# Kernel optimization log

Measured on AMD Instinct MI355X. Metric: run time of the kernel, lower is better.

The kernel has to match this reference:

```python
import jax, jax.numpy as jnp
import numpy as np

D_MODEL = 1024
D_STATE = 128
D_CONV = 4
EXPAND = 2
HEADDIM = 64
NGROUPS = 1
CHUNK = 256
D_INNER = EXPAND * D_MODEL          # 2048
NHEADS = D_INNER // HEADDIM         # 32
D_IN_PROJ = 2 * D_INNER + 2 * NGROUPS * D_STATE + NHEADS  # 4384
CONV_DIM = D_INNER + 2 * NGROUPS * D_STATE                # 2304
BATCH, SEQLEN = 2, 2048


def rmsnorm(x, w, eps=1e-6):
    ms = jnp.mean(x * x, axis=-1, keepdims=True)
    return w * (x * jax.lax.rsqrt(ms + eps))


def layernorm(x, eps=1e-5):
    mu = jnp.mean(x, axis=-1, keepdims=True)
    var = jnp.mean((x - mu) ** 2, axis=-1, keepdims=True)
    return (x - mu) * jax.lax.rsqrt(var + eps)


def activation_quant(x):
    # int8-style fake quant with STE, scale differentiable (matches torch)
    amax = jnp.clip(jnp.max(jnp.abs(x), axis=-1, keepdims=True), 1e-5, None)
    scale = 127.0 / amax
    q = jnp.clip(jnp.round(x * scale), -128, 127)
    return (jax.lax.stop_gradient(q - x * scale) + x * scale) / scale


def weight_quant(w):
    # ternary {-1,0,1}; note: NOT rescaled by scale (matches the triton kernel)
    scale = jnp.clip(jnp.mean(jnp.abs(w)), 1e-5, None)
    wq = jnp.clip(jnp.round(w / scale), -1.0, 1.0)
    return w + jax.lax.stop_gradient(wq - w)  # STE: identity grad


def bitlinear(x, w):
    return activation_quant(layernorm(x)) @ weight_quant(w).T


def segsum(x):
    # x: [..., T] -> [..., T, T] lower-triangular cumulative segment sums
    T = x.shape[-1]
    cs = jnp.cumsum(x, axis=-1)
    ss = cs[..., :, None] - cs[..., None, :]
    mask = jnp.tril(jnp.ones((T, T), dtype=bool))
    return jnp.where(mask, ss, -jnp.inf)


def ssd(u, a, B, C, chunk):
    # u: b l h p (= x*dt); a: b l h (= A*dt); B, C: b l h n (per-head)
    b, l, h, p = u.shape
    n = B.shape[-1]
    c = l // chunk
    u = u.reshape(b, c, chunk, h, p)
    a = a.reshape(b, c, chunk, h).transpose(0, 3, 1, 2)   # b h c s
    B = B.reshape(b, c, chunk, h, n)
    C = C.reshape(b, c, chunk, h, n)
    a_cs = jnp.cumsum(a, axis=-1)                          # b h c s
    L = jnp.exp(segsum(a))                                 # b h c s s
    Y_diag = jnp.einsum('bclhn,bcshn,bhcls,bcshp->bclhp', C, B, L, u)
    decay_states = jnp.exp(a_cs[..., -1:] - a_cs)          # b h c s
    states = jnp.einsum('bclhn,bhcl,bclhp->bchpn', B, decay_states, u)
    a_chunk = jnp.pad(a_cs[..., -1], ((0, 0), (0, 0), (1, 0)))  # b h (c+1)
    decay_chunk = jnp.exp(segsum(a_chunk))                 # b h (c+1) (c+1)
    states = jnp.concatenate([jnp.zeros_like(states[:, :1]), states], axis=1)
    new_states = jnp.einsum('bhzc,bchpn->bzhpn', decay_chunk, states)
    prev_states = new_states[:, :-1]                       # state entering each chunk
    Y_off = jnp.einsum('bclhn,bchpn,bhcl->bclhp', C, prev_states, jnp.exp(a_cs))
    return (Y_diag + Y_off).reshape(b, l, h, p)


def setup_inputs() -> dict:
    key = jax.random.key(0)
    ks = jax.random.split(key, 6)
    hidden_states = jax.random.normal(ks[0], (BATCH, SEQLEN, D_MODEL), jnp.float32)
    in_proj_w = jax.random.normal(ks[1], (D_IN_PROJ, D_MODEL), jnp.float32) / np.sqrt(D_MODEL).astype(np.float32)
    out_proj_w = jax.random.normal(ks[2], (D_MODEL, D_INNER), jnp.float32) / np.sqrt(D_INNER).astype(np.float32)
    conv_w = jax.random.normal(ks[3], (CONV_DIM, D_CONV), jnp.float32) * 0.1
    conv_b = jnp.zeros((CONV_DIM,), jnp.float32)
    A_log = jnp.log(jnp.arange(1, NHEADS + 1, dtype=jnp.float32))
    Dp = jnp.ones((NHEADS,), jnp.float32)
    dt_min, dt_max, dt_floor = 1e-3, 1e-1, 1e-4
    inv_dt = jnp.exp(jax.random.uniform(ks[4], (NHEADS,)) * (np.log(dt_max) - np.log(dt_min)) + np.log(dt_min))
    inv_dt = jnp.clip(inv_dt, dt_floor, None)
    dt_bias = inv_dt + jnp.log(-jnp.expm1(-inv_dt))
    norm_w = jnp.ones((D_MODEL,), jnp.float32)
    out_norm_w = jnp.ones((D_INNER,), jnp.float32)
    return dict(hidden_states=hidden_states, norm_w=norm_w, in_proj_w=in_proj_w,
                conv_w=conv_w, conv_b=conv_b, A_log=A_log, Dp=Dp, dt_bias=dt_bias,
                out_norm_w=out_norm_w, out_proj_w=out_proj_w)


def reference(hidden_states, norm_w, in_proj_w, conv_w, conv_b, A_log, Dp, dt_bias, out_norm_w, out_proj_w):
    b, l, _ = hidden_states.shape
    h = rmsnorm(hidden_states, norm_w)
    zxbcdt = bitlinear(h, in_proj_w)                       # b l (2*d_inner + 2*g*n + h)
    z = zxbcdt[..., :D_INNER]
    xBC = zxbcdt[..., D_INNER:D_INNER + CONV_DIM]
    dt = zxbcdt[..., D_INNER + CONV_DIM:]                  # b l h
    # causal depthwise conv1d (kernel D_CONV) + silu
    xp = jnp.pad(xBC, ((0, 0), (D_CONV - 1, 0), (0, 0)))
    conv = sum(xp[:, k:k + l, :] * conv_w[:, k] for k in range(D_CONV)) + conv_b
    xBC = jax.nn.silu(conv)
    x = xBC[..., :D_INNER].reshape(b, l, NHEADS, HEADDIM)
    Bm = xBC[..., D_INNER:D_INNER + NGROUPS * D_STATE].reshape(b, l, NGROUPS, D_STATE)
    Cm = xBC[..., D_INNER + NGROUPS * D_STATE:].reshape(b, l, NGROUPS, D_STATE)
    hpg = NHEADS // NGROUPS
    Bh = jnp.repeat(Bm, hpg, axis=2)                       # b l h n
    Ch = jnp.repeat(Cm, hpg, axis=2)
    dt = jax.nn.softplus(dt + dt_bias)                     # dt_softplus=True
    A = -jnp.exp(A_log)
    y = ssd(x * dt[..., None], dt * A, Bh, Ch, CHUNK)      # b l h p
    y = y + x * Dp[None, None, :, None]                    # D skip
    y = y * jax.nn.silu(z).reshape(b, l, NHEADS, HEADDIM)  # z gate
    y = rmsnorm(y.reshape(b, l, D_INNER), out_norm_w)
    out = bitlinear(y, out_proj_w)
    return hidden_states + out
```

## Files before the change

### kernel.cpp

```cpp
#include <hip/hip_runtime.h>
#include <stdint.h>
#include <stddef.h>
#include <math.h>

#define TOKS 4096
#define DM   1024
#define DIP  4384
#define DI   2048
#define CVD  2304
#define NH   32
#define HD   64
#define DST  128
#define NCH  8
#define CHK  256

typedef int v4i  __attribute__((ext_vector_type(4)));
typedef int v16i __attribute__((ext_vector_type(16)));
typedef short s8v __attribute__((ext_vector_type(8)));
typedef float f16v __attribute__((ext_vector_type(16)));
typedef unsigned short ushort_t;

static const size_t OFF_ZX    = 0;
static const size_t OFF_SX    = OFF_ZX + (size_t)TOKS*DIP*4;
static const size_t OFF_ST    = OFF_SX + (size_t)TOKS*CVD*4;
static const size_t OFF_YG    = OFF_ST + (size_t)512*HD*DST*4;
static const size_t OFF_Q1    = OFF_YG + (size_t)TOKS*DI*4;
static const size_t OFF_Q2    = OFF_Q1 + (size_t)TOKS*DM;
static const size_t OFF_WQ1   = OFF_Q2 + (size_t)TOKS*DI;
static const size_t OFF_WQ2   = OFF_WQ1 + (size_t)DIP*DM;
static const size_t OFF_RS1   = OFF_WQ2 + (size_t)DM*DI;
static const size_t OFF_RS2   = OFF_RS1 + (size_t)TOKS*4;
static const size_t OFF_DT    = OFF_RS2 + (size_t)TOKS*4;
static const size_t OFF_ACS   = OFF_DT + (size_t)TOKS*NH*4;
static const size_t OFF_CSUM  = OFF_ACS + (size_t)512*CHK*8;
static const size_t OFF_PART  = OFF_CSUM + 512*8;
static const size_t OFF_WSC   = OFF_PART + 1024*8;
static const size_t OFF_BH    = OFF_WSC + 64;
static const size_t OFF_BL    = OFF_BH  + (size_t)TOKS*128*2;
static const size_t OFF_CHG   = OFF_BL  + (size_t)TOKS*128*2;
static const size_t OFF_CLG   = OFF_CHG + (size_t)TOKS*128*2;
static const size_t OFF_GRAM  = OFF_CLG + (size_t)TOKS*128*2;
static const size_t OFF_UTH   = OFF_GRAM + (size_t)16*256*256*4;
static const size_t OFF_UTL   = OFF_UTH + (size_t)512*64*256*2;
static const size_t OFF_PH    = OFF_UTL + (size_t)512*64*256*2;
static const size_t OFF_PL    = OFF_PH  + (size_t)512*64*128*2;

__device__ __forceinline__ ushort_t f2bf(float x) {
  union { float f; unsigned int u; } v; v.f = x;
  unsigned int r = v.u + 0x7FFFu + ((v.u >> 16) & 1u);
  return (ushort_t)(r >> 16);
}
__device__ __forceinline__ float bf2f(ushort_t h) {
  union { unsigned int u; float f; } v; v.u = ((unsigned int)h) << 16;
  return v.f;
}

__device__ __forceinline__ double bsumd(double v, double* sb) {
#pragma unroll
  for (int o = 32; o; o >>= 1) v += __shfl_down(v, o);
  int lane = threadIdx.x & 63, w = threadIdx.x >> 6;
  __syncthreads();
  if (lane == 0) sb[w] = v;
  __syncthreads();
  return sb[0] + sb[1] + sb[2] + sb[3];
}
__device__ __forceinline__ double bmaxd(double v, double* sb) {
#pragma unroll
  for (int o = 32; o; o >>= 1) v = fmax(v, __shfl_down(v, o));
  int lane = threadIdx.x & 63, w = threadIdx.x >> 6;
  __syncthreads();
  if (lane == 0) sb[w] = v;
  __syncthreads();
  return fmax(fmax(sb[0], sb[1]), fmax(sb[2], sb[3]));
}
__device__ __forceinline__ void bsum3d(double& a, double& b, double& c, double* sb) {
#pragma unroll
  for (int o = 32; o; o >>= 1) {
    a += __shfl_down(a, o);
    b += __shfl_down(b, o);
    c += __shfl_down(c, o);
  }
  int lane = threadIdx.x & 63, w = threadIdx.x >> 6;
  __syncthreads();
  if (lane == 0) { sb[w * 3 + 0] = a; sb[w * 3 + 1] = b; sb[w * 3 + 2] = c; }
  __syncthreads();
  a = sb[0] + sb[3] + sb[6] + sb[9];
  b = sb[1] + sb[4] + sb[7] + sb[10];
  c = sb[2] + sb[5] + sb[8] + sb[11];
}

__global__ void __launch_bounds__(256) k_absmean(const float* __restrict__ w, int n, double* __restrict__ part) {
  double s = 0.0;
  for (int i = blockIdx.x * 256 + threadIdx.x; i < n; i += 512 * 256) s += (double)fabsf(w[i]);
  __shared__ double sb[4];
  s = bsumd(s, sb);
  if (threadIdx.x == 0) part[blockIdx.x] = s;
}

__global__ void __launch_bounds__(256) k_wscale(const double* __restrict__ part, double* __restrict__ wsc, int n1, int n2) {
  __shared__ double sb[4];
  double s = part[threadIdx.x] + part[threadIdx.x + 256];
  double t1 = bsumd(s, sb);
  __syncthreads();
  s = part[512 + threadIdx.x] + part[512 + threadIdx.x + 256];
  double t2 = bsumd(s, sb);
  if (threadIdx.x == 0) {
    wsc[0] = fmax(t1 / (double)n1, 1e-5);
    wsc[1] = fmax(t2 / (double)n2, 1e-5);
  }
}

__global__ void __launch_bounds__(256) k_tern(const float* __restrict__ w, int n, const double* __restrict__ wsc, int which, int8_t* __restrict__ out) {
  int i = blockIdx.x * 256 + threadIdx.x;
  if (i < n) {
    double sc = wsc[which];
    double q = fmin(fmax(rint((double)w[i] / sc), -1.0), 1.0);
    out[i] = (int8_t)q;
  }
}

template <int D>
__global__ void __launch_bounds__(256) k_normquant(const float* __restrict__ in, const float* __restrict__ w,
                                                   int8_t* __restrict__ q, float* __restrict__ rs) {
  constexpr int E = D / 256;
  int t = blockIdx.x, tid = threadIdx.x;
  const float* row = in + (size_t)t * D;
  __shared__ double sb[12];
  double y[E];
  double s0 = 0.0, s1 = 0.0, s2 = 0.0;
#pragma unroll
  for (int i = 0; i < E; i++) {
    double xv = (double)row[tid + 256 * i];
    double wv = (double)w[tid + 256 * i];
    s0 += xv * xv;
    double yy = wv * xv;
    y[i] = yy;
    s1 += yy;
    s2 += yy * yy;
  }
  bsum3d(s0, s1, s2, sb);
  double rr = 1.0 / sqrt(s0 / (double)D + 1e-6);
  double mu = rr * (s1 / (double)D);
  double var = rr * rr * (s2 / (double)D) - mu * mu;
  double rv = 1.0 / sqrt(var + 1e-5);
  double M = 0.0;
#pragma unroll
  for (int i = 0; i < E; i++) { y[i] = y[i] * rr - mu; M = fmax(M, fabs(y[i])); }
  M = bmaxd(M, sb);
  double am = fmax(M * rv, 1e-5);
  double sc = 127.0 / am;
#pragma unroll
  for (int i = 0; i < E; i++) {
    double qq = fmin(fmax(rint(y[i] * rv * sc), -128.0), 127.0);
    q[(size_t)t * D + tid + 256 * i] = (int8_t)qq;
  }
  if (tid == 0) rs[t] = (float)(am / 127.0);
}

__global__ void __launch_bounds__(256, 3) k_gemm_mfma(const int8_t* __restrict__ A, const int8_t* __restrict__ W,
                                                      const float* __restrict__ rs, const float* __restrict__ addend,
                                                      float* __restrict__ out, int M, int N, int K) {
  __shared__ int8_t Al[128 * 80];
  __shared__ int8_t Bl[128 * 80];
  int m0 = blockIdx.x * 128, n0 = blockIdx.y * 128;
  int t = threadIdx.x;
  int w = t >> 6, lane = t & 63;
  int wm = w >> 1, wn = w & 1;
  int l31 = lane & 31, lh = lane >> 5;

  v16i acc[2][2] = {};

  for (int k0 = 0; k0 < K; k0 += 64) {
    __syncthreads();
#pragma unroll
    for (int it = 0; it < 2; ++it) {
      int c = t + 256 * it;
      int row = c >> 2, kc = (c & 3) * 16;
      int4 av = *(const int4*)(A + (size_t)(m0 + row) * K + k0 + kc);
      *(int4*)(Al + row * 80 + kc) = av;
      int4 bv;
      if (n0 + row < N) bv = *(const int4*)(W + (size_t)(n0 + row) * K + k0 + kc);
      else { bv.x = bv.y = bv.z = bv.w = 0; }
      *(int4*)(Bl + row * 80 + kc) = bv;
    }
    __syncthreads();
#pragma unroll
    for (int ks = 0; ks < 2; ++ks) {
      v4i af[2], bf[2];
#pragma unroll
      for (int tm = 0; tm < 2; ++tm)
        af[tm] = *(const v4i*)(Al + (wm * 64 + tm * 32 + l31) * 80 + ks * 32 + lh * 16);
#pragma unroll
      for (int tn = 0; tn < 2; ++tn)
        bf[tn] = *(const v4i*)(Bl + (wn * 64 + tn * 32 + l31) * 80 + ks * 32 + lh * 16);
#pragma unroll
      for (int tm = 0; tm < 2; ++tm)
#pragma unroll
        for (int tn = 0; tn < 2; ++tn)
          acc[tm][tn] = __builtin_amdgcn_mfma_i32_32x32x32_i8(af[tm], bf[tn], acc[tm][tn], 0, 0, 0);
    }
  }

#pragma unroll
  for (int tm = 0; tm < 2; ++tm)
#pragma unroll
    for (int tn = 0; tn < 2; ++tn) {
      int n = n0 + wn * 64 + tn * 32 + l31;
      if (n < N) {
#pragma unroll
        for (int r = 0; r < 16; ++r) {
          int mrel = (r & 3) + 8 * (r >> 2) + 4 * lh;
          int m = m0 + wm * 64 + tm * 32 + mrel;
          float v = rs[m] * (float)acc[tm][tn][r];
          if (addend) v += addend[(size_t)m * N + n];
          out[(size_t)m * N + n] = v;
        }
      }
    }
}

__global__ void __launch_bounds__(256) k_conv(const float* __restrict__ zx, const float* __restrict__ cw,
                                              const float* __restrict__ cb, float* __restrict__ sx,
                                              ushort_t* __restrict__ bh2, ushort_t* __restrict__ bl2,
                                              ushort_t* __restrict__ ch2, ushort_t* __restrict__ cl2) {
  int c = blockIdx.x * 256 + threadIdx.x;
  int t = blockIdx.y;
  int b = t >> 11, l = t & 2047;
  float acc = cb[c];
#pragma unroll
  for (int k = 0; k < 4; k++) {
    int li = l - 3 + k;
    if (li >= 0) acc = fmaf(zx[(size_t)(b * 2048 + li) * DIP + DI + c], cw[c * 4 + k], acc);
  }
  float val = acc / (1.f + expf(-acc));
  sx[(size_t)t * CVD + c] = val;
  if (c >= DI) {
    int idx = c - DI;
    ushort_t hh = f2bf(val);
    ushort_t ll = f2bf(val - bf2f(hh));
    int bc = t >> 8, lt = (t >> 5) & 7, l31 = t & 31;
    int n = idx & 127;
    int ks = n >> 4, lhf = (n >> 3) & 1, j = n & 7;
    size_t o = ((((size_t)(bc * 8 + lt) * 8 + ks) * 2 + lhf) * 32 + l31) * 8 + j;
    if (idx < 128) { bh2[o] = hh; bl2[o] = ll; }
    else           { ch2[o] = hh; cl2[o] = ll; }
  }
}

__global__ void __launch_bounds__(256) k_cumsum(const float* __restrict__ zx, const float* __restrict__ dt_bias,
                                                const float* __restrict__ A_log, float* __restrict__ dtv,
                                                double* __restrict__ acs, double* __restrict__ csum) {
  int bid = blockIdx.x;
  int h = bid & 31, bc = bid >> 5;
  int s = threadIdx.x;
  int tok = bc * 256 + s;
  float x = zx[(size_t)tok * DIP + (DI + CVD) + h] + dt_bias[h];
  float dt = fmaxf(x, 0.f) + log1pf(expf(-fabsf(x)));
  dtv[(size_t)tok * 32 + h] = dt;
  double negA = -exp((double)A_log[h]);
  double a = (double)dt * negA;
  __shared__ double buf[256];
  buf[s] = a;
  __syncthreads();
  for (int o = 1; o < 256; o <<= 1) {
    double add = (s >= o) ? buf[s - o] : 0.0;
    __syncthreads();
    buf[s] += add;
    __syncthreads();
  }
  acs[(size_t)bid * 256 + s] = buf[s];
  if (s == 255) csum[bid] = buf[s];
}

__global__ void __launch_bounds__(256) k_gram(const ushort_t* __restrict__ bh2, const ushort_t* __restrict__ bl2,
                                              const ushort_t* __restrict__ ch2, const ushort_t* __restrict__ cl2,
                                              float* __restrict__ gr2) {
  int blk = blockIdx.x;
  int bc = blk >> 3, lt = blk & 7;
  int t = threadIdx.x;
  int w = t >> 6, lane = t & 63;
  int l31 = lane & 31, lhf = lane >> 5;
  __shared__ float Gl[4][32 * 36];

  s8v ch[8], cl[8];
#pragma unroll
  for (int ks = 0; ks < 8; ++ks) {
    size_t ca = ((((size_t)(bc * 8 + lt) * 8 + ks) * 2 + lhf) * 32 + l31) * 8;
    ch[ks] = *(const s8v*)(ch2 + ca);
    cl[ks] = *(const s8v*)(cl2 + ca);
  }
  for (int st = w; st <= lt; st += 4) {
    f16v acc = {};
#pragma unroll
    for (int ks = 0; ks < 8; ++ks) {
      size_t ba = ((((size_t)(bc * 8 + st) * 8 + ks) * 2 + lhf) * 32 + l31) * 8;
      s8v bh = *(const s8v*)(bh2 + ba);
      s8v bl = *(const s8v*)(bl2 + ba);
      acc = __builtin_amdgcn_mfma_f32_32x32x16_bf16(ch[ks], bh, acc, 0, 0, 0);
      acc = __builtin_amdgcn_mfma_f32_32x32x16_bf16(ch[ks], bl, acc, 0, 0, 0);
      acc = __builtin_amdgcn_mfma_f32_32x32x16_bf16(cl[ks], bh, acc, 0, 0, 0);
    }
#pragma unroll
    for (int rr = 0; rr < 16; ++rr) {
      int lrow = (rr & 3) + 8 * (rr >> 2) + 4 * lhf;
      Gl[w][lrow * 36 + l31] = acc[rr];
    }
#pragma unroll
    for (int i2 = 0; i2 < 2; ++i2) {
      int idx = i2 * 2 + lhf;
      int k2g = idx >> 1, lhf2 = idx & 1;
      size_t gb = ((((size_t)(bc * 8 + lt) * 8 + st) * 2 + k2g) * 2 + lhf2) * 256 + l31 * 8;
      float4 a = *(const float4*)(&Gl[w][l31 * 36 + k2g * 16 + lhf2 * 8]);
      float4 b = *(const float4*)(&Gl[w][l31 * 36 + k2g * 16 + lhf2 * 8 + 4]);
      *(float4*)(gr2 + gb) = a;
      *(float4*)(gr2 + gb + 4) = b;
    }
  }
}

__global__ void __launch_bounds__(256) k_prepuT(const float* __restrict__ sx, const float* __restrict__ dtv,
                                                ushort_t* __restrict__ uth2, ushort_t* __restrict__ utl2) {
  int r = blockIdx.x;
  int h = r & 31, bc = r >> 5;
  int t = threadIdx.x;
  __shared__ float Xs[64 * 68];
  __shared__ float dts[64];
  for (int slab = 0; slab < 4; ++slab) {
    int s0 = slab * 64;
    if (slab) __syncthreads();
    if (t < 64) dts[t] = dtv[(size_t)(bc * 256 + s0 + t) * 32 + h];
    {
      int s = t >> 2, pg = (t & 3) * 16;
      const float* xr = sx + (size_t)(bc * 256 + s0 + s) * CVD + h * 64 + pg;
      float* dst = &Xs[s * 68 + pg];
#pragma unroll
      for (int i = 0; i < 4; ++i)
        *(float4*)(dst + i * 4) = *(const float4*)(xr + i * 4);
    }
    __syncthreads();
#pragma unroll
    for (int half = 0; half < 2; ++half) {
      int it = t + half * 256;
      int l31 = it & 31, g = it >> 5;
      int stl = g >> 3, k2 = (g >> 2) & 1, pt = (g >> 1) & 1, lhf = g & 1;
      int p = pt * 32 + l31;
      int sb = stl * 32 + k2 * 16 + lhf * 8;
      union { int4 q; ushort_t e[8]; } H, L;
#pragma unroll
      for (int j = 0; j < 8; ++j) {
        float f = Xs[(sb + j) * 68 + p] * dts[sb + j];
        ushort_t hh = f2bf(f);
        H.e[j] = hh;
        L.e[j] = f2bf(f - bf2f(hh));
      }
      int st = slab * 2 + stl;
      size_t base = (((((size_t)r * 8 + st) * 2 + k2) * 2 + pt) * 2 + lhf) * 256 + l31 * 8;
      *(int4*)(uth2 + base) = H.q;
      *(int4*)(utl2 + base) = L.q;
    }
  }
}

__global__ void __launch_bounds__(256, 4) k_states2(const float* __restrict__ sx, const float* __restrict__ dtv,
                                                    const double* __restrict__ acs, const double* __restrict__ csum,
                                                    float* __restrict__ states) {
  int r = blockIdx.x;
  int h = r & 31, bc = r >> 5;
  int t = threadIdx.x, tx = t & 15, ty = t >> 4;
  __shared__ float du[64 * 68];
  double last = csum[r];
  float acc[4][8] = {};
  for (int s0 = 0; s0 < 256; s0 += 64) {
    __syncthreads();
    {
      int s = t >> 2, pg = (t & 3) * 16;
      int tok = bc * 256 + s0 + s;
      float w = expf((float)(last - acs[(size_t)r * 256 + s0 + s])) * dtv[(size_t)tok * 32 + h];
      const float* xr = sx + (size_t)tok * CVD + h * 64 + pg;
      float* dst = &du[s * 68 + pg];
#pragma unroll
      for (int i = 0; i < 4; i++) {
        float4 v = *(const float4*)(xr + i * 4);
        v.x *= w; v.y *= w; v.z *= w; v.w *= w;
        *(float4*)(dst + i * 4) = v;
      }
    }
    __syncthreads();
#pragma unroll 4
    for (int s = 0; s < 64; s++) {
      int tok = bc * 256 + s0 + s;
      const float* br = sx + (size_t)tok * CVD + DI + ty * 8;
      float4 b0 = *(const float4*)(br);
      float4 b1 = *(const float4*)(br + 4);
      float4 d4 = *(const float4*)(&du[s * 68 + tx * 4]);
      float dd[4] = {d4.x, d4.y, d4.z, d4.w};
      float bv[8] = {b0.x, b0.y, b0.z, b0.w, b1.x, b1.y, b1.z, b1.w};
#pragma unroll
      for (int i = 0; i < 4; i++)
#pragma unroll
        for (int j = 0; j < 8; j++) acc[i][j] = fmaf(dd[i], bv[j], acc[i][j]);
    }
  }
  size_t base = (size_t)r * (HD * DST);
#pragma unroll
  for (int i = 0; i < 4; i++) {
    float4 v0, v1;
    v0.x = acc[i][0]; v0.y = acc[i][1]; v0.z = acc[i][2]; v0.w = acc[i][3];
    v1.x = acc[i][4]; v1.y = acc[i][5]; v1.z = acc[i][6]; v1.w = acc[i][7];
    *(float4*)(states + base + (size_t)(tx * 4 + i) * DST + ty * 8) = v0;
    *(float4*)(states + base + (size_t)(tx * 4 + i) * DST + ty * 8 + 4) = v1;
  }
}

__global__ void __launch_bounds__(256) k_chunkscan(float* __restrict__ states, const double* __restrict__ csum,
                                                   ushort_t* __restrict__ ph2, ushort_t* __restrict__ pl2) {
  int idx = blockIdx.x * 256 + threadIdx.x;
  int n = idx & 127, p = (idx >> 7) & 63, h = (idx >> 13) & 31, b = idx >> 18;
  int ks = n >> 4, lhf = (n >> 3) & 1, j = n & 7, pt = p >> 5, l31 = p & 31;
  float Nv = 0.f;
  for (int c = 0; c < 8; c++) {
    int bid = (b * 8 + c) * 32 + h;
    size_t addr = (size_t)bid * (HD * DST) + p * DST + n;
    float s = states[addr];
    states[addr] = Nv;
    ushort_t hh = f2bf(Nv);
    size_t o = (((((size_t)bid * 8 + ks) * 2 + pt) * 2 + lhf) * 32 + l31) * 8 + j;
    ph2[o] = hh;
    pl2[o] = f2bf(Nv - bf2f(hh));
    Nv = Nv * expf((float)csum[bid]) + s;
  }
}

__global__ void __launch_bounds__(64) k_y9(const float* __restrict__ sx, const double* __restrict__ acs,
                                           const ushort_t* __restrict__ ch2, const ushort_t* __restrict__ cl2,
                                           const ushort_t* __restrict__ ph2, const ushort_t* __restrict__ pl2,
                                           const float* __restrict__ gr2,
                                           const ushort_t* __restrict__ uth2, const ushort_t* __restrict__ utl2,
                                           const float* __restrict__ zx, const float* __restrict__ Dp,
                                           float* __restrict__ yg) {
  int myid = (blockIdx.x & 7) * 512 + (blockIdx.x >> 3);
  int r = myid >> 3, lt = myid & 7;
  int h = r & 31, bc = r >> 5;
  int lane = threadIdx.x;
  int l31 = lane & 31, lhf = lane >> 5;
  int lw = lt * 32;
  int lg = lw + l31;
  const double* acsr = acs + (size_t)r * 256;
  double a_l = acsr[lg];

  f16v Yacc[2] = {};
#pragma unroll
  for (int ks = 0; ks < 8; ++ks) {
    size_t ca = ((((size_t)(bc * 8 + lt) * 8 + ks) * 2 + lhf) * 32 + l31) * 8;
    s8v ch = *(const s8v*)(ch2 + ca);
    s8v cl = *(const s8v*)(cl2 + ca);
#pragma unroll
    for (int pt = 0; pt < 2; ++pt) {
      size_t pa = (((((size_t)r * 8 + ks) * 2 + pt) * 2 + lhf) * 32 + l31) * 8;
      s8v ph = *(const s8v*)(ph2 + pa);
      s8v pl = *(const s8v*)(pl2 + pa);
      Yacc[pt] = __builtin_amdgcn_mfma_f32_32x32x16_bf16(ch, ph, Yacc[pt], 0, 0, 0);
      Yacc[pt] = __builtin_amdgcn_mfma_f32_32x32x16_bf16(ch, pl, Yacc[pt], 0, 0, 0);
      Yacc[pt] = __builtin_amdgcn_mfma_f32_32x32x16_bf16(cl, ph, Yacc[pt], 0, 0, 0);
    }
  }
#pragma unroll
  for (int rr = 0; rr < 16; ++rr) {
    int lrow = (rr & 3) + 8 * (rr >> 2) + 4 * lhf;
    float el = expf((float)acsr[lw + lrow]);
    Yacc[0][rr] *= el;
    Yacc[1][rr] *= el;
  }

  for (int st = 0; st <= lt; ++st) {
#pragma unroll
    for (int k2 = 0; k2 < 2; ++k2) {
      size_t gb = (((((size_t)(bc * 8 + lt) * 8 + st) * 2 + k2) * 2 + lhf) * 256) + l31 * 8;
      float4 g0 = *(const float4*)(gr2 + gb);
      float4 g1 = *(const float4*)(gr2 + gb + 4);
      float gv[8] = {g0.x, g0.y, g0.z, g0.w, g1.x, g1.y, g1.z, g1.w};
      int sbase = st * 32 + k2 * 16 + lhf * 8;
      union { s8v v; ushort_t e[8]; } AH, AL;
#pragma unroll
      for (int j = 0; j < 8; ++j) {
        float v = 0.f;
        if (sbase + j <= lg) v = expf((float)(a_l - acsr[sbase + j])) * gv[j];
        ushort_t hh = f2bf(v);
        AH.e[j] = hh;
        AL.e[j] = f2bf(v - bf2f(hh));
      }
#pragma unroll
      for (int pt = 0; pt < 2; ++pt) {
        size_t ub = ((((((size_t)r * 8 + st) * 2 + k2) * 2 + pt) * 2 + lhf) * 256) + l31 * 8;
        s8v uh = *(const s8v*)(uth2 + ub);
        s8v ul = *(const s8v*)(utl2 + ub);
        Yacc[pt] = __builtin_amdgcn_mfma_f32_32x32x16_bf16(AH.v, uh, Yacc[pt], 0, 0, 0);
        Yacc[pt] = __builtin_amdgcn_mfma_f32_32x32x16_bf16(AH.v, ul, Yacc[pt], 0, 0, 0);
        Yacc[pt] = __builtin_amdgcn_mfma_f32_32x32x16_bf16(AL.v, uh, Yacc[pt], 0, 0, 0);
      }
    }
  }

  float dph = Dp[h];
#pragma unroll
  for (int pt = 0; pt < 2; ++pt) {
    int p = pt * 32 + l31;
#pragma unroll
    for (int rr = 0; rr < 16; ++rr) {
      int lrow = (rr & 3) + 8 * (rr >> 2) + 4 * lhf;
      size_t tok = (size_t)(bc * 256 + lw + lrow);
      float xv = sx[tok * CVD + h * 64 + p];
      float zv = zx[tok * DIP + h * 64 + p];
      float y = (Yacc[pt][rr] + xv * dph) * (zv / (1.f + expf(-zv)));
      yg[tok * DI + h * 64 + p] = y;
    }
  }
}

extern "C" void kernel_launch(void* const* d_in, const int* in_sizes, int n_in,
                              void* d_out, int out_size, void* d_ws, size_t ws_size,
                              hipStream_t stream) {
  const float* hidden   = (const float*)d_in[0];
  const float* norm_w   = (const float*)d_in[1];
  const float* in_proj  = (const float*)d_in[2];
  const float* conv_w   = (const float*)d_in[3];
  const float* conv_b   = (const float*)d_in[4];
  const float* A_log    = (const float*)d_in[5];
  const float* Dp       = (const float*)d_in[6];
  const float* dt_bias  = (const float*)d_in[7];
  const float* out_norm = (const float*)d_in[8];
  const float* out_proj = (const float*)d_in[9];
  float* out = (float*)d_out;

  char* ws = (char*)d_ws;
  float*  zx    = (float*)(ws + OFF_ZX);
  float*  sx    = (float*)(ws + OFF_SX);
  float*  st    = (float*)(ws + OFF_ST);
  float*  yg    = (float*)(ws + OFF_YG);
  int8_t* q1    = (int8_t*)(ws + OFF_Q1);
  int8_t* q2    = (int8_t*)(ws + OFF_Q2);
  int8_t* wq1   = (int8_t*)(ws + OFF_WQ1);
  int8_t* wq2   = (int8_t*)(ws + OFF_WQ2);
  float*  rs1   = (float*)(ws + OFF_RS1);
  float*  rs2   = (float*)(ws + OFF_RS2);
  float*  dtv   = (float*)(ws + OFF_DT);
  double* acs   = (double*)(ws + OFF_ACS);
  double* csum  = (double*)(ws + OFF_CSUM);
  double* part  = (double*)(ws + OFF_PART);
  double* wsc   = (double*)(ws + OFF_WSC);
  ushort_t* bh2 = (ushort_t*)(ws + OFF_BH);
  ushort_t* bl2 = (ushort_t*)(ws + OFF_BL);
  ushort_t* ch2 = (ushort_t*)(ws + OFF_CHG);
  ushort_t* cl2 = (ushort_t*)(ws + OFF_CLG);
  float*  gr2   = (float*)(ws + OFF_GRAM);
  ushort_t* uth2 = (ushort_t*)(ws + OFF_UTH);
  ushort_t* utl2 = (ushort_t*)(ws + OFF_UTL);
  ushort_t* ph2 = (ushort_t*)(ws + OFF_PH);
  ushort_t* pl2 = (ushort_t*)(ws + OFF_PL);

  const int n1 = DIP * DM, n2 = DM * DI;

  hipLaunchKernelGGL(k_absmean, dim3(512), dim3(256), 0, stream, in_proj, n1, part);
  hipLaunchKernelGGL(k_absmean, dim3(512), dim3(256), 0, stream, out_proj, n2, part + 512);
  hipLaunchKernelGGL(k_wscale, dim3(1), dim3(256), 0, stream, part, wsc, n1, n2);
  hipLaunchKernelGGL(k_tern, dim3((n1 + 255) / 256), dim3(256), 0, stream, in_proj, n1, wsc, 0, wq1);
  hipLaunchKernelGGL(k_tern, dim3((n2 + 255) / 256), dim3(256), 0, stream, out_proj, n2, wsc, 1, wq2);
  hipLaunchKernelGGL(k_normquant<DM>, dim3(TOKS), dim3(256), 0, stream, hidden, norm_w, q1, rs1);
  hipLaunchKernelGGL(k_gemm_mfma, dim3(TOKS / 128, (DIP + 127) / 128), dim3(256), 0, stream,
                     q1, wq1, rs1, (const float*)nullptr, zx, TOKS, DIP, DM);
  hipLaunchKernelGGL(k_conv, dim3(CVD / 256, TOKS), dim3(256), 0, stream, zx, conv_w, conv_b, sx,
                     bh2, bl2, ch2, cl2);
  hipLaunchKernelGGL(k_cumsum, dim3(512), dim3(256), 0, stream, zx, dt_bias, A_log, dtv, acs, csum);
  hipLaunchKernelGGL(k_gram, dim3(128), dim3(256), 0, stream, bh2, bl2, ch2, cl2, gr2);
  hipLaunchKernelGGL(k_prepuT, dim3(512), dim3(256), 0, stream, sx, dtv, uth2, utl2);
  hipLaunchKernelGGL(k_states2, dim3(512), dim3(256), 0, stream, sx, dtv, acs, csum, st);
  hipLaunchKernelGGL(k_chunkscan, dim3(2 * NH * HD * DST / 256), dim3(256), 0, stream, st, csum, ph2, pl2);
  hipLaunchKernelGGL(k_y9, dim3(4096), dim3(64), 0, stream, sx, acs, ch2, cl2, ph2, pl2, gr2, uth2, utl2, zx, Dp, yg);
  hipLaunchKernelGGL(k_normquant<DI>, dim3(TOKS), dim3(256), 0, stream, yg, out_norm, q2, rs2);
  hipLaunchKernelGGL(k_gemm_mfma, dim3(TOKS / 128, DM / 128), dim3(256), 0, stream,
                     q2, wq2, rs2, hidden, out, TOKS, DM, DI);
  (void)in_sizes; (void)n_in; (void)out_size; (void)ws_size;
}
```

Measured before the change: 381.9 us.

## Split Y kernel by p-tile across waves and pair triangular chunk rows

The Y-output kernel now runs 128-thread blocks in which each wave handles one 32-column p-tile instead of one wave doing both. Each block processes two l-tiles (lt and 7-lt), so the triangular intra-chunk loop gives every block the same total work. This targets load imbalance from the triangular loop and low per-wave parallelism. In exchange, each wave recomputes the decay/gram A-fragments that the old single wave shared across both p-tiles, and the two l-tiles inside a block run one after the other.

```diff
diff --git a/kernel.cpp b/kernel.cpp
--- a/kernel.cpp
+++ b/kernel.cpp
@@ -431,79 +431,74 @@
   }
 }
 
-__global__ void __launch_bounds__(64) k_y9(const float* __restrict__ sx, const double* __restrict__ acs,
-                                           const ushort_t* __restrict__ ch2, const ushort_t* __restrict__ cl2,
-                                           const ushort_t* __restrict__ ph2, const ushort_t* __restrict__ pl2,
-                                           const float* __restrict__ gr2,
-                                           const ushort_t* __restrict__ uth2, const ushort_t* __restrict__ utl2,
-                                           const float* __restrict__ zx, const float* __restrict__ Dp,
-                                           float* __restrict__ yg) {
-  int myid = (blockIdx.x & 7) * 512 + (blockIdx.x >> 3);
-  int r = myid >> 3, lt = myid & 7;
+__global__ void __launch_bounds__(128) k_y10(const float* __restrict__ sx, const double* __restrict__ acs,
+                                             const ushort_t* __restrict__ ch2, const ushort_t* __restrict__ cl2,
+                                             const ushort_t* __restrict__ ph2, const ushort_t* __restrict__ pl2,
+                                             const float* __restrict__ gr2,
+                                             const ushort_t* __restrict__ uth2, const ushort_t* __restrict__ utl2,
+                                             const float* __restrict__ zx, const float* __restrict__ Dp,
+                                             float* __restrict__ yg) {
+  int myid = (blockIdx.x & 7) * 256 + (blockIdx.x >> 3);
+  int r = myid >> 2, pair = myid & 3;
   int h = r & 31, bc = r >> 5;
-  int lane = threadIdx.x;
+  int pt = threadIdx.x >> 6;
+  int lane = threadIdx.x & 63;
   int l31 = lane & 31, lhf = lane >> 5;
-  int lw = lt * 32;
-  int lg = lw + l31;
   const double* acsr = acs + (size_t)r * 256;
-  double a_l = acsr[lg];
-
-  f16v Yacc[2] = {};
-#pragma unroll
-  for (int ks = 0; ks < 8; ++ks) {
-    size_t ca = ((((size_t)(bc * 8 + lt) * 8 + ks) * 2 + lhf) * 32 + l31) * 8;
-    s8v ch = *(const s8v*)(ch2 + ca);
-    s8v cl = *(const s8v*)(cl2 + ca);
-#pragma unroll
-    for (int pt = 0; pt < 2; ++pt) {
+  float dph = Dp[h];
+
+#pragma unroll
+  for (int sel = 0; sel < 2; ++sel) {
+    int lt = sel ? (7 - pair) : pair;
+    int lw = lt * 32;
+    int lg = lw + l31;
+    double a_l = acsr[lg];
+
+    f16v Yacc = {};
+#pragma unroll
+    for (int ks = 0; ks < 8; ++ks) {
+      size_t ca = ((((size_t)(bc * 8 + lt) * 8 + ks) * 2 + lhf) * 32 + l31) * 8;
+      s8v ch = *(const s8v*)(ch2 + ca);
+      s8v cl = *(const s8v*)(cl2 + ca);
       size_t pa = (((((size_t)r * 8 + ks) * 2 + pt) * 2 + lhf) * 32 + l31) * 8;
       s8v ph = *(const s8v*)(ph2 + pa);
       s8v pl = *(const s8v*)(pl2 + pa);
-      Yacc[pt] = __builtin_amdgcn_mfma_f32_32x32x16_bf16(ch, ph, Yacc[pt], 0, 0, 0);
-      Yacc[pt] = __builtin_amdgcn_mfma_f32_32x32x16_bf16(ch, pl, Yacc[pt], 0, 0, 0);
-      Yacc[pt] = __builtin_amdgcn_mfma_f32_32x32x16_bf16(cl, ph, Yacc[pt], 0, 0, 0);
-    }
-  }
-#pragma unroll
-  for (int rr = 0; rr < 16; ++rr) {
-    int lrow = (rr & 3) + 8 * (rr >> 2) + 4 * lhf;
-    float el = expf((float)acsr[lw + lrow]);
-    Yacc[0][rr] *= el;
-    Yacc[1][rr] *= el;
-  }
-
-  for (int st = 0; st <= lt; ++st) {
-#pragma unroll
-    for (int k2 = 0; k2 < 2; ++k2) {
-      size_t gb = (((((size_t)(bc * 8 + lt) * 8 + st) * 2 + k2) * 2 + lhf) * 256) + l31 * 8;
-      float4 g0 = *(const float4*)(gr2 + gb);
-      float4 g1 = *(const float4*)(gr2 + gb + 4);
-      float gv[8] = {g0.x, g0.y, g0.z, g0.w, g1.x, g1.y, g1.z, g1.w};
-      int sbase = st * 32 + k2 * 16 + lhf * 8;
-      union { s8v v; ushort_t e[8]; } AH, AL;
-#pragma unroll
-      for (int j = 0; j < 8; ++j) {
-        float v = 0.f;
-        if (sbase + j <= lg) v = expf((float)(a_l - acsr[sbase + j])) * gv[j];
-        ushort_t hh = f2bf(v);
-        AH.e[j] = hh;
-        AL.e[j] = f2bf(v - bf2f(hh));
-      }
-#pragma unroll
-      for (int pt = 0; pt < 2; ++pt) {
+      Yacc = __builtin_amdgcn_mfma_f32_32x32x16_bf16(ch, ph, Yacc, 0, 0, 0);
+      Yacc = __builtin_amdgcn_mfma_f32_32x32x16_bf16(ch, pl, Yacc, 0, 0, 0);
+      Yacc = __builtin_amdgcn_mfma_f32_32x32x16_bf16(cl, ph, Yacc, 0, 0, 0);
+    }
+#pragma unroll
+    for (int rr = 0; rr < 16; ++rr) {
+      int lrow = (rr & 3) + 8 * (rr >> 2) + 4 * lhf;
+      Yacc[rr] *= expf((float)acsr[lw + lrow]);
+    }
+
+    for (int st = 0; st <= lt; ++st) {
+#pragma unroll
+      for (int k2 = 0; k2 < 2; ++k2) {
+        size_t gb = (((((size_t)(bc * 8 + lt) * 8 + st) * 2 + k2) * 2 + lhf) * 256) + l31 * 8;
+        float4 g0 = *(const float4*)(gr2 + gb);
+        float4 g1 = *(const float4*)(gr2 + gb + 4);
+        float gv[8] = {g0.x, g0.y, g0.z, g0.w, g1.x, g1.y, g1.z, g1.w};
+        int sbase = st * 32 + k2 * 16 + lhf * 8;
+        union { s8v v; ushort_t e[8]; } AH, AL;
+#pragma unroll
+        for (int j = 0; j < 8; ++j) {
+          float v = 0.f;
+          if (sbase + j <= lg) v = expf((float)(a_l - acsr[sbase + j])) * gv[j];
+          ushort_t hh = f2bf(v);
+          AH.e[j] = hh;
+          AL.e[j] = f2bf(v - bf2f(hh));
+        }
         size_t ub = ((((((size_t)r * 8 + st) * 2 + k2) * 2 + pt) * 2 + lhf) * 256) + l31 * 8;
         s8v uh = *(const s8v*)(uth2 + ub);
         s8v ul = *(const s8v*)(utl2 + ub);
-        Yacc[pt] = __builtin_amdgcn_mfma_f32_32x32x16_bf16(AH.v, uh, Yacc[pt], 0, 0, 0);
-        Yacc[pt] = __builtin_amdgcn_mfma_f32_32x32x16_bf16(AH.v, ul, Yacc[pt], 0, 0, 0);
-        Yacc[pt] = __builtin_amdgcn_mfma_f32_32x32x16_bf16(AL.v, uh, Yacc[pt], 0, 0, 0);
+        Yacc = __builtin_amdgcn_mfma_f32_32x32x16_bf16(AH.v, uh, Yacc, 0, 0, 0);
+        Yacc = __builtin_amdgcn_mfma_f32_32x32x16_bf16(AH.v, ul, Yacc, 0, 0, 0);
+        Yacc = __builtin_amdgcn_mfma_f32_32x32x16_bf16(AL.v, uh, Yacc, 0, 0, 0);
       }
     }
-  }
-
-  float dph = Dp[h];
-#pragma unroll
-  for (int pt = 0; pt < 2; ++pt) {
+
     int p = pt * 32 + l31;
 #pragma unroll
     for (int rr = 0; rr < 16; ++rr) {
@@ -511,7 +506,7 @@
       size_t tok = (size_t)(bc * 256 + lw + lrow);
       float xv = sx[tok * CVD + h * 64 + p];
       float zv = zx[tok * DIP + h * 64 + p];
-      float y = (Yacc[pt][rr] + xv * dph) * (zv / (1.f + expf(-zv)));
+      float y = (Yacc[rr] + xv * dph) * (zv / (1.f + expf(-zv)));
       yg[tok * DI + h * 64 + p] = y;
     }
   }
@@ -575,7 +570,7 @@
   hipLaunchKernelGGL(k_prepuT, dim3(512), dim3(256), 0, stream, sx, dtv, uth2, utl2);
   hipLaunchKernelGGL(k_states2, dim3(512), dim3(256), 0, stream, sx, dtv, acs, csum, st);
   hipLaunchKernelGGL(k_chunkscan, dim3(2 * NH * HD * DST / 256), dim3(256), 0, stream, st, csum, ph2, pl2);
-  hipLaunchKernelGGL(k_y9, dim3(4096), dim3(64), 0, stream, sx, acs, ch2, cl2, ph2, pl2, gr2, uth2, utl2, zx, Dp, yg);
+  hipLaunchKernelGGL(k_y10, dim3(2048), dim3(128), 0, stream, sx, acs, ch2, cl2, ph2, pl2, gr2, uth2, utl2, zx, Dp, yg);
   hipLaunchKernelGGL(k_normquant<DI>, dim3(TOKS), dim3(256), 0, stream, yg, out_norm, q2, rs2);
   hipLaunchKernelGGL(k_gemm_mfma, dim3(TOKS / 128, DM / 128), dim3(256), 0, stream,
                      q2, wq2, rs2, hidden, out, TOKS, DM, DI);
```

Result: slower. 405.2 us (+6.1%).

## Compute chunk states with split-bf16 MFMA using pre-laid-out transposed B

Applied to the files above, without the earlier changes.

Replaces the FP32 FMA-based chunk-state kernel with one built on bf16 MFMA 32x32x16 instructions. It reuses the hi/lo-split u^T tiles already produced for the Y kernel, and adds a transposed hi/lo copy of B written by the conv kernel in MFMA operand layout. Decay weights are applied to B per step and re-split into bf16 hi/lo, with three MFMAs per tile to keep near-fp32 accuracy. This trades scalar FMA work and strided global reads of sx for matrix-core throughput, at the cost of extra workspace, extra scattered writes in k_conv and slightly different rounding.

```diff
diff --git a/kernel.cpp b/kernel.cpp
--- a/kernel.cpp
+++ b/kernel.cpp
@@ -44,6 +44,8 @@
 static const size_t OFF_UTL   = OFF_UTH + (size_t)512*64*256*2;
 static const size_t OFF_PH    = OFF_UTL + (size_t)512*64*256*2;
 static const size_t OFF_PL    = OFF_PH  + (size_t)512*64*128*2;
+static const size_t OFF_BTH   = OFF_PL + (size_t)512*64*128*2;
+static const size_t OFF_BTL   = OFF_BTH + (size_t)16*4*16*2*32*8*2;
 
 __device__ __forceinline__ ushort_t f2bf(float x) {
   union { float f; unsigned int u; } v; v.f = x;
@@ -222,7 +224,8 @@
 __global__ void __launch_bounds__(256) k_conv(const float* __restrict__ zx, const float* __restrict__ cw,
                                               const float* __restrict__ cb, float* __restrict__ sx,
                                               ushort_t* __restrict__ bh2, ushort_t* __restrict__ bl2,
-                                              ushort_t* __restrict__ ch2, ushort_t* __restrict__ cl2) {
+                                              ushort_t* __restrict__ ch2, ushort_t* __restrict__ cl2,
+                                              ushort_t* __restrict__ bth, ushort_t* __restrict__ btl) {
   int c = blockIdx.x * 256 + threadIdx.x;
   int t = blockIdx.y;
   int b = t >> 11, l = t & 2047;
@@ -242,8 +245,16 @@
     int n = idx & 127;
     int ks = n >> 4, lhf = (n >> 3) & 1, j = n & 7;
     size_t o = ((((size_t)(bc * 8 + lt) * 8 + ks) * 2 + lhf) * 32 + l31) * 8 + j;
-    if (idx < 128) { bh2[o] = hh; bl2[o] = ll; }
-    else           { ch2[o] = hh; cl2[o] = ll; }
+    if (idx < 128) {
+      bh2[o] = hh; bl2[o] = ll;
+      int s = t & 255;
+      int nt = n >> 5, n31 = n & 31;
+      int kg = s >> 4, lhf2 = (s >> 3) & 1, j2 = s & 7;
+      size_t o2 = ((((size_t)(bc * 4 + nt) * 16 + kg) * 2 + lhf2) * 32 + n31) * 8 + j2;
+      bth[o2] = hh; btl[o2] = ll;
+    } else {
+      ch2[o] = hh; cl2[o] = ll;
+    }
   }
 }
 
@@ -361,54 +372,61 @@
   }
 }
 
-__global__ void __launch_bounds__(256, 4) k_states2(const float* __restrict__ sx, const float* __restrict__ dtv,
-                                                    const double* __restrict__ acs, const double* __restrict__ csum,
-                                                    float* __restrict__ states) {
+__global__ void __launch_bounds__(256) k_states3(const ushort_t* __restrict__ uth2, const ushort_t* __restrict__ utl2,
+                                                 const ushort_t* __restrict__ bth, const ushort_t* __restrict__ btl,
+                                                 const double* __restrict__ acs, const double* __restrict__ csum,
+                                                 float* __restrict__ states) {
   int r = blockIdx.x;
-  int h = r & 31, bc = r >> 5;
-  int t = threadIdx.x, tx = t & 15, ty = t >> 4;
-  __shared__ float du[64 * 68];
-  double last = csum[r];
-  float acc[4][8] = {};
-  for (int s0 = 0; s0 < 256; s0 += 64) {
-    __syncthreads();
-    {
-      int s = t >> 2, pg = (t & 3) * 16;
-      int tok = bc * 256 + s0 + s;
-      float w = expf((float)(last - acs[(size_t)r * 256 + s0 + s])) * dtv[(size_t)tok * 32 + h];
-      const float* xr = sx + (size_t)tok * CVD + h * 64 + pg;
-      float* dst = &du[s * 68 + pg];
-#pragma unroll
-      for (int i = 0; i < 4; i++) {
-        float4 v = *(const float4*)(xr + i * 4);
-        v.x *= w; v.y *= w; v.z *= w; v.w *= w;
-        *(float4*)(dst + i * 4) = v;
+  int bc = r >> 5;
+  int t = threadIdx.x, w = t >> 6, lane = t & 63;
+  int n31 = lane & 31, lhf = lane >> 5;
+  int pt = w & 1, nt0 = w >> 1;
+  __shared__ float wd[256];
+  {
+    double last = csum[r];
+    wd[t] = expf((float)(last - acs[(size_t)r * 256 + t]));
+  }
+  __syncthreads();
+
+  f16v acc0 = {}, acc1 = {};
+  for (int kg = 0; kg < 16; ++kg) {
+    int st = kg >> 1, k2 = kg & 1;
+    size_t ua = (((((size_t)r * 8 + st) * 2 + k2) * 2 + pt) * 2 + lhf) * 256 + n31 * 8;
+    s8v ah = *(const s8v*)(uth2 + ua);
+    s8v al = *(const s8v*)(utl2 + ua);
+#pragma unroll
+    for (int half = 0; half < 2; ++half) {
+      int nt = nt0 + half * 2;
+      size_t ba = ((((size_t)(bc * 4 + nt) * 16 + kg) * 2 + lhf) * 32 + n31) * 8;
+      s8v bh = *(const s8v*)(bth + ba);
+      s8v bl = *(const s8v*)(btl + ba);
+      union { s8v v; ushort_t e[8]; } BH, BL;
+#pragma unroll
+      for (int j = 0; j < 8; ++j) {
+        int s = kg * 16 + lhf * 8 + j;
+        float bv = (bf2f((ushort_t)bh[j]) + bf2f((ushort_t)bl[j])) * wd[s];
+        ushort_t hh = f2bf(bv);
+        BH.e[j] = hh;
+        BL.e[j] = f2bf(bv - bf2f(hh));
       }
-    }
-    __syncthreads();
-#pragma unroll 4
-    for (int s = 0; s < 64; s++) {
-      int tok = bc * 256 + s0 + s;
-      const float* br = sx + (size_t)tok * CVD + DI + ty * 8;
-      float4 b0 = *(const float4*)(br);
-      float4 b1 = *(const float4*)(br + 4);
-      float4 d4 = *(const float4*)(&du[s * 68 + tx * 4]);
-      float dd[4] = {d4.x, d4.y, d4.z, d4.w};
-      float bv[8] = {b0.x, b0.y, b0.z, b0.w, b1.x, b1.y, b1.z, b1.w};
-#pragma unroll
-      for (int i = 0; i < 4; i++)
-#pragma unroll
-        for (int j = 0; j < 8; j++) acc[i][j] = fmaf(dd[i], bv[j], acc[i][j]);
+      if (half == 0) {
+        acc0 = __builtin_amdgcn_mfma_f32_32x32x16_bf16(ah, BH.v, acc0, 0, 0, 0);
+        acc0 = __builtin_amdgcn_mfma_f32_32x32x16_bf16(ah, BL.v, acc0, 0, 0, 0);
+        acc0 = __builtin_amdgcn_mfma_f32_32x32x16_bf16(al, BH.v, acc0, 0, 0, 0);
+      } else {
+        acc1 = __builtin_amdgcn_mfma_f32_32x32x16_bf16(ah, BH.v, acc1, 0, 0, 0);
+        acc1 = __builtin_amdgcn_mfma_f32_32x32x16_bf16(ah, BL.v, acc1, 0, 0, 0);
+        acc1 = __builtin_amdgcn_mfma_f32_32x32x16_bf16(al, BH.v, acc1, 0, 0, 0);
+      }
     }
   }
   size_t base = (size_t)r * (HD * DST);
 #pragma unroll
-  for (int i = 0; i < 4; i++) {
-    float4 v0, v1;
-    v0.x = acc[i][0]; v0.y = acc[i][1]; v0.z = acc[i][2]; v0.w = acc[i][3];
-    v1.x = acc[i][4]; v1.y = acc[i][5]; v1.z = acc[i][6]; v1.w = acc[i][7];
-    *(float4*)(states + base + (size_t)(tx * 4 + i) * DST + ty * 8) = v0;
-    *(float4*)(states + base + (size_t)(tx * 4 + i) * DST + ty * 8 + 4) = v1;
+  for (int rr = 0; rr < 16; ++rr) {
+    int prel = (rr & 3) + 8 * (rr >> 2) + 4 * lhf;
+    int p = pt * 32 + prel;
+    states[base + (size_t)p * DST + nt0 * 32 + n31] = acc0[rr];
+    states[base + (size_t)p * DST + (nt0 + 2) * 32 + n31] = acc1[rr];
   }
 }
 
@@ -557,6 +575,8 @@
   ushort_t* utl2 = (ushort_t*)(ws + OFF_UTL);
   ushort_t* ph2 = (ushort_t*)(ws + OFF_PH);
   ushort_t* pl2 = (ushort_t*)(ws + OFF_PL);
+  ushort_t* bth = (ushort_t*)(ws + OFF_BTH);
+  ushort_t* btl = (ushort_t*)(ws + OFF_BTL);
 
   const int n1 = DIP * DM, n2 = DM * DI;
 
@@ -569,11 +589,11 @@
   hipLaunchKernelGGL(k_gemm_mfma, dim3(TOKS / 128, (DIP + 127) / 128), dim3(256), 0, stream,
                      q1, wq1, rs1, (const float*)nullptr, zx, TOKS, DIP, DM);
   hipLaunchKernelGGL(k_conv, dim3(CVD / 256, TOKS), dim3(256), 0, stream, zx, conv_w, conv_b, sx,
-                     bh2, bl2, ch2, cl2);
+                     bh2, bl2, ch2, cl2, bth, btl);
   hipLaunchKernelGGL(k_cumsum, dim3(512), dim3(256), 0, stream, zx, dt_bias, A_log, dtv, acs, csum);
   hipLaunchKernelGGL(k_gram, dim3(128), dim3(256), 0, stream, bh2, bl2, ch2, cl2, gr2);
   hipLaunchKernelGGL(k_prepuT, dim3(512), dim3(256), 0, stream, sx, dtv, uth2, utl2);
-  hipLaunchKernelGGL(k_states2, dim3(512), dim3(256), 0, stream, sx, dtv, acs, csum, st);
+  hipLaunchKernelGGL(k_states3, dim3(512), dim3(256), 0, stream, uth2, utl2, bth, btl, acs, csum, st);
   hipLaunchKernelGGL(k_chunkscan, dim3(2 * NH * HD * DST / 256), dim3(256), 0, stream, st, csum, ph2, pl2);
   hipLaunchKernelGGL(k_y9, dim3(4096), dim3(64), 0, stream, sx, acs, ch2, cl2, ph2, pl2, gr2, uth2, utl2, zx, Dp, yg);
   hipLaunchKernelGGL(k_normquant<DI>, dim3(TOKS), dim3(256), 0, stream, yg, out_norm, q2, rs2);
```

Result: faster. 353.8 us (-7.4%).
